# Kernel tuning notes

Measured on AMD Instinct MI355X. Metric: run time of the kernel, lower is better.

Reference implementation:

```python
import jax, jax.numpy as jnp
import numpy as np

L, H, K, N_IN, B = 8, 512, 16, 512, 8192  # layers, nodes/layer, fan-in, input nodes, batch


def setup_inputs() -> dict:
    key = jax.random.key(0)
    k_x, k_w, k_b = jax.random.split(key, 3)
    x = jax.random.normal(k_x, (B, N_IN), dtype=jnp.float32)
    # DAG links: node in layer l may read any of the N_IN + l*H previously computed nodes
    rng = np.random.default_rng(0)
    link_idx = np.stack(
        [rng.integers(0, N_IN + l * H, size=(H, K)) for l in range(L)]
    ).astype(np.int32)  # [L, H, K]
    weights = jax.random.normal(k_w, (L, H, K), dtype=jnp.float32) * 0.3
    bias = jax.random.normal(k_b, (L, H), dtype=jnp.float32) * 0.1
    return {"x": x, "link_idx": jnp.asarray(link_idx), "weights": weights, "bias": bias}


def reference(x, link_idx, weights, bias):
    # values dict -> growing [B, n_nodes_so_far] buffer; per-node Linear(K,1)+Sigmoid
    values = x  # [B, N_IN]
    for l in range(L):  # small fixed structural loop over topological layers
        g = values[:, link_idx[l]]                      # gather predecessor values [B, H, K]
        out = jax.nn.sigmoid(
            jnp.einsum("bhk,hk->bh", g, weights[l]) + bias[l]
        )                                               # [B, H]
        values = jnp.concatenate([values, out], axis=1)
    return values[:, -H:]  # output nodes = last layer
```

## Files before the change

### kernel.cpp

```cpp
#include <hip/hip_runtime.h>
#include <hip/hip_fp16.h>

#define LAYERS 8
#define H      512
#define K      16
#define N_IN   512
#define BATCH  8192
#define R      8
#define NT     512
#define LDS_COLS 4096

__global__ __launch_bounds__(NT, 4)
void ffn_fused_kernel(const float* __restrict__ x,
                      const int*   __restrict__ link_idx,
                      const float* __restrict__ weights,
                      const float* __restrict__ bias,
                      float*       __restrict__ out)
{
    __shared__ __align__(16) __half vals[LDS_COLS * R];

    const int tid  = threadIdx.x;
    const int row0 = blockIdx.x * R;

    {
        const int c = tid;
        float v[R];
        #pragma unroll
        for (int r = 0; r < R; ++r)
            v[r] = x[(row0 + r) * N_IN + c];
        __half2 p[R / 2];
        #pragma unroll
        for (int r = 0; r < R / 2; ++r)
            p[r] = __floats2half2_rn(v[2 * r], v[2 * r + 1]);
        *(uint4*)&vals[c * R] = *(const uint4*)p;
    }
    __syncthreads();

    for (int l = 0; l < LAYERS; ++l) {
        const int h    = tid;
        const int base = (l * H + h) * K;
        int   idx[K];
        float w[K];
        #pragma unroll
        for (int q = 0; q < 4; ++q) {
            *(int4*)  &idx[4 * q] = ((const int4*)  (link_idx + base))[q];
            *(float4*)&w  [4 * q] = ((const float4*)(weights  + base))[q];
        }
        const float b = bias[l * H + h];
        float acc[R];
        #pragma unroll
        for (int r = 0; r < R; ++r) acc[r] = b;

        #pragma unroll
        for (int k = 0; k < K; ++k) {
            const uint4 g = *(const uint4*)&vals[idx[k] * R];
            const __half2* hp = (const __half2*)&g;
            const float wk = w[k];
            #pragma unroll
            for (int r = 0; r < R / 2; ++r) {
                const float2 f = __half22float2(hp[r]);
                acc[2 * r]     = fmaf(f.x, wk, acc[2 * r]);
                acc[2 * r + 1] = fmaf(f.y, wk, acc[2 * r + 1]);
            }
        }

        #pragma unroll
        for (int r = 0; r < R; ++r)
            acc[r] = 1.0f / (1.0f + __expf(-acc[r]));

        if (l < LAYERS - 1) {
            __half2 p[R / 2];
            #pragma unroll
            for (int r = 0; r < R / 2; ++r)
                p[r] = __floats2half2_rn(acc[2 * r], acc[2 * r + 1]);
            *(uint4*)&vals[(N_IN + l * H + h) * R] = *(const uint4*)p;
            __syncthreads();
        } else {
            #pragma unroll
            for (int r = 0; r < R; ++r)
                out[(row0 + r) * H + h] = acc[r];
        }
    }
}

extern "C" void kernel_launch(void* const* d_in, const int* in_sizes, int n_in,
                              void* d_out, int out_size, void* d_ws, size_t ws_size,
                              hipStream_t stream) {
    const float* x        = (const float*)d_in[0];
    const int*   link_idx = (const int*)  d_in[1];
    const float* weights  = (const float*)d_in[2];
    const float* bias     = (const float*)d_in[3];
    float*       out      = (float*)d_out;

    ffn_fused_kernel<<<dim3(BATCH / R), dim3(NT), 0, stream>>>(x, link_idx, weights, bias, out);
}
```

Measured before the change: 115.9 us.

## Split each node's fan-in across two lanes with DPP reduction, 1024 threads

Each output node is now handled by a pair of lanes, each summing half of the 16 fan-in links, with partial sums combined through a DPP quad-permute swap. Each lane then applies the sigmoid and writes only 4 of the 8 batch rows. The block grows to 1024 threads to double the parallelism per block and hide LDS gather latency. In exchange it doubles the thread count against the same 64KB LDS and halves the work each lane does, so occupancy and register pressure change and there is extra cross-lane traffic.

New measurement: 142.6 us. 1.23x slower.

```diff
diff --git a/kernel.cpp b/kernel.cpp
--- a/kernel.cpp
+++ b/kernel.cpp
@@ -7,10 +7,15 @@
 #define N_IN   512
 #define BATCH  8192
 #define R      8
-#define NT     512
+#define NT     1024
 #define LDS_COLS 4096
 
-__global__ __launch_bounds__(NT, 4)
+__device__ __forceinline__ float dpp_xor1(float x) {
+    return __int_as_float(__builtin_amdgcn_update_dpp(
+        0, __float_as_int(x), 0xB1, 0xF, 0xF, true));
+}
+
+__global__ __launch_bounds__(NT, 8)
 void ffn_fused_kernel(const float* __restrict__ x,
                       const int*   __restrict__ link_idx,
                       const float* __restrict__ weights,
@@ -20,39 +25,38 @@
     __shared__ __align__(16) __half vals[LDS_COLS * R];
 
     const int tid  = threadIdx.x;
+    const int h    = tid >> 1;
+    const int half = tid & 1;
     const int row0 = blockIdx.x * R;
 
     {
-        const int c = tid;
-        float v[R];
+        float v[4];
         #pragma unroll
-        for (int r = 0; r < R; ++r)
-            v[r] = x[(row0 + r) * N_IN + c];
-        __half2 p[R / 2];
-        #pragma unroll
-        for (int r = 0; r < R / 2; ++r)
-            p[r] = __floats2half2_rn(v[2 * r], v[2 * r + 1]);
-        *(uint4*)&vals[c * R] = *(const uint4*)p;
+        for (int j = 0; j < 4; ++j)
+            v[j] = x[(row0 + half * 4 + j) * N_IN + h];
+        __half2 p[2];
+        p[0] = __floats2half2_rn(v[0], v[1]);
+        p[1] = __floats2half2_rn(v[2], v[3]);
+        *(uint2*)&vals[h * R + half * 4] = *(const uint2*)p;
     }
     __syncthreads();
 
     for (int l = 0; l < LAYERS; ++l) {
-        const int h    = tid;
-        const int base = (l * H + h) * K;
-        int   idx[K];
-        float w[K];
-        #pragma unroll
-        for (int q = 0; q < 4; ++q) {
-            *(int4*)  &idx[4 * q] = ((const int4*)  (link_idx + base))[q];
-            *(float4*)&w  [4 * q] = ((const float4*)(weights  + base))[q];
-        }
-        const float b = bias[l * H + h];
+        const int base = (l * H + h) * K + half * 8;
+        int   idx[8];
+        float w[8];
+        *(int4*)  &idx[0] = ((const int4*)  (link_idx + base))[0];
+        *(int4*)  &idx[4] = ((const int4*)  (link_idx + base))[1];
+        *(float4*)&w[0]   = ((const float4*)(weights  + base))[0];
+        *(float4*)&w[4]   = ((const float4*)(weights  + base))[1];
+
+        const float b = half ? 0.0f : bias[l * H + h];
         float acc[R];
         #pragma unroll
         for (int r = 0; r < R; ++r) acc[r] = b;
 
         #pragma unroll
-        for (int k = 0; k < K; ++k) {
+        for (int k = 0; k < 8; ++k) {
             const uint4 g = *(const uint4*)&vals[idx[k] * R];
             const __half2* hp = (const __half2*)&g;
             const float wk = w[k];
@@ -64,21 +68,28 @@
             }
         }
 
+        float t[R];
         #pragma unroll
         for (int r = 0; r < R; ++r)
-            acc[r] = 1.0f / (1.0f + __expf(-acc[r]));
+            t[r] = acc[r] + dpp_xor1(acc[r]);
+
+        float o[4];
+        #pragma unroll
+        for (int j = 0; j < 4; ++j) {
+            const float s = half ? t[4 + j] : t[j];
+            o[j] = 1.0f / (1.0f + __expf(-s));
+        }
 
         if (l < LAYERS - 1) {
-            __half2 p[R / 2];
-            #pragma unroll
-            for (int r = 0; r < R / 2; ++r)
-                p[r] = __floats2half2_rn(acc[2 * r], acc[2 * r + 1]);
-            *(uint4*)&vals[(N_IN + l * H + h) * R] = *(const uint4*)p;
+            __half2 p[2];
+            p[0] = __floats2half2_rn(o[0], o[1]);
+            p[1] = __floats2half2_rn(o[2], o[3]);
+            *(uint2*)&vals[(N_IN + l * H + h) * R + half * 4] = *(const uint2*)p;
             __syncthreads();
         } else {
             #pragma unroll
-            for (int r = 0; r < R; ++r)
-                out[(row0 + r) * H + h] = acc[r];
+            for (int j = 0; j < 4; ++j)
+                out[(row0 + half * 4 + j) * H + h] = o[j];
         }
     }
 }
```

## Prefetch next layer's links and weights during compute; use fast reciprocal in sigmoid

Applied to the files above, without the earlier changes.

Each layer's link indices, weights and bias are now loaded one layer ahead into registers and rotated at the barrier, so global-load latency overlaps the current layer's LDS gathers and FMAs. The layer loop is fully unrolled. Launch bounds are relaxed from 4 to 2 blocks per CU to leave room for the extra registers. The sigmoid division is replaced by the hardware reciprocal builtin, which is slightly less accurate and may lower occupancy.

Measured after the change: 109.4 us. 5.6% less time.

```diff
diff --git a/kernel.cpp b/kernel.cpp
--- a/kernel.cpp
+++ b/kernel.cpp
@@ -10,7 +10,8 @@
 #define NT     512
 #define LDS_COLS 4096
 
-__global__ __launch_bounds__(NT, 4)
+
+__global__ __launch_bounds__(NT, 2)
 void ffn_fused_kernel(const float* __restrict__ x,
                       const int*   __restrict__ link_idx,
                       const float* __restrict__ weights,
@@ -34,28 +35,42 @@
             p[r] = __floats2half2_rn(v[2 * r], v[2 * r + 1]);
         *(uint4*)&vals[c * R] = *(const uint4*)p;
     }
+
+    int   idxA[K]; float wA[K]; float bA;
+    {
+        const int base = tid * K;
+        #pragma unroll
+        for (int q = 0; q < 4; ++q) {
+            *(int4*)  &idxA[4 * q] = ((const int4*)  (link_idx + base))[q];
+            *(float4*)&wA  [4 * q] = ((const float4*)(weights  + base))[q];
+        }
+        bA = bias[tid];
+    }
+
     __syncthreads();
 
+    #pragma unroll
     for (int l = 0; l < LAYERS; ++l) {
-        const int h    = tid;
-        const int base = (l * H + h) * K;
-        int   idx[K];
-        float w[K];
-        #pragma unroll
-        for (int q = 0; q < 4; ++q) {
-            *(int4*)  &idx[4 * q] = ((const int4*)  (link_idx + base))[q];
-            *(float4*)&w  [4 * q] = ((const float4*)(weights  + base))[q];
+        int idxB[K]; float wB[K]; float bB = 0.0f;
+        if (l < LAYERS - 1) {
+            const int nb = ((l + 1) * H + tid) * K;
+            #pragma unroll
+            for (int q = 0; q < 4; ++q) {
+                *(int4*)  &idxB[4 * q] = ((const int4*)  (link_idx + nb))[q];
+                *(float4*)&wB  [4 * q] = ((const float4*)(weights  + nb))[q];
+            }
+            bB = bias[(l + 1) * H + tid];
         }
-        const float b = bias[l * H + h];
+
         float acc[R];
         #pragma unroll
-        for (int r = 0; r < R; ++r) acc[r] = b;
+        for (int r = 0; r < R; ++r) acc[r] = bA;
 
         #pragma unroll
         for (int k = 0; k < K; ++k) {
-            const uint4 g = *(const uint4*)&vals[idx[k] * R];
+            const uint4 g = *(const uint4*)&vals[idxA[k] * R];
             const __half2* hp = (const __half2*)&g;
-            const float wk = w[k];
+            const float wk = wA[k];
             #pragma unroll
             for (int r = 0; r < R / 2; ++r) {
                 const float2 f = __half22float2(hp[r]);
@@ -66,19 +81,22 @@
 
         #pragma unroll
         for (int r = 0; r < R; ++r)
-            acc[r] = 1.0f / (1.0f + __expf(-acc[r]));
+            acc[r] = __builtin_amdgcn_rcpf(1.0f + __expf(-acc[r]));
 
         if (l < LAYERS - 1) {
             __half2 p[R / 2];
             #pragma unroll
             for (int r = 0; r < R / 2; ++r)
                 p[r] = __floats2half2_rn(acc[2 * r], acc[2 * r + 1]);
-            *(uint4*)&vals[(N_IN + l * H + h) * R] = *(const uint4*)p;
+            *(uint4*)&vals[(N_IN + l * H + tid) * R] = *(const uint4*)p;
             __syncthreads();
+            #pragma unroll
+            for (int k = 0; k < K; ++k) { idxA[k] = idxB[k]; wA[k] = wB[k]; }
+            bA = bB;
         } else {
             #pragma unroll
             for (int r = 0; r < R; ++r)
-                out[(row0 + r) * H + h] = acc[r];
+                out[(row0 + r) * H + tid] = acc[r];
         }
     }
 }
```
